# Kernel optimization log

Measured on AMD Instinct MI355X. Metric: run time of the kernel, lower is better.

## Reference

```python
import jax, jax.numpy as jnp
import numpy as np
import math

C, NH, HD, L, P, FFN = 256, 8, 32, 1, 4, 512
H_BEV, W_BEV = 200, 100
NQ, BS, NV = 1000, 4, H_BEV * W_BEV
EPS = 1e-5


def _ln(x, g, b):
    m = x.mean(-1, keepdims=True)
    v = ((x - m) ** 2).mean(-1, keepdims=True)
    return (x - m) / jnp.sqrt(v + EPS) * g + b


def _mha(x, qpos, in_w, in_b, ow, ob):
    # nn.MultiheadAttention self-attention; key_pos = query_pos (shapes match)
    q = x + qpos
    k = x + qpos
    v = x
    wq, wk, wv = jnp.split(in_w, 3, axis=0)
    bq, bk, bv = jnp.split(in_b, 3, axis=0)
    bs, nq, _ = x.shape
    qh = (q @ wq.T + bq).reshape(bs, nq, NH, HD)
    kh = (k @ wk.T + bk).reshape(bs, nq, NH, HD)
    vh = (v @ wv.T + bv).reshape(bs, nq, NH, HD)
    scores = jnp.einsum('bqhd,bkhd->bhqk', qh, kh) / jnp.sqrt(jnp.float32(HD))
    attn = jax.nn.softmax(scores, axis=-1)
    out = jnp.einsum('bhqk,bkhd->bqhd', attn, vh).reshape(bs, nq, C)
    return out @ ow.T + ob


def _msdeform(x, qpos, value, ref, spatial_shapes, so_w, so_b, aw_w, aw_b, vp_w, vp_b, op_w, op_b):
    # Multi-scale deformable attention (single level), bilinear sampling with
    # align_corners=False convention and zero padding, as in the CUDA kernel.
    bs, nq, _ = x.shape
    q = x + qpos
    v = (value @ vp_w.T + vp_b).reshape(bs, NV, NH, HD).transpose(0, 2, 1, 3)  # [bs,nh,nv,hd]
    off = (q @ so_w.T + so_b).reshape(bs, nq, NH, L, P, 2)
    aw = jax.nn.softmax((q @ aw_w.T + aw_b).reshape(bs, nq, NH, L * P), axis=-1)
    aw = aw.reshape(bs, nq, NH, L, P)
    norm = jnp.stack([spatial_shapes[:, 1], spatial_shapes[:, 0]], -1).astype(jnp.float32)  # [L,2] = (W,H)
    loc = ref[:, :, None, :, None, :] + off / norm[None, None, None, :, None, :]  # [bs,nq,nh,L,P,2]
    loc = loc[:, :, :, 0]  # single level -> [bs,nq,nh,P,2]
    awp = aw[:, :, :, 0]   # [bs,nq,nh,P]
    x_im = loc[..., 0] * W_BEV - 0.5
    y_im = loc[..., 1] * H_BEV - 0.5
    x0 = jnp.floor(x_im)
    y0 = jnp.floor(y_im)
    lx = x_im - x0
    ly = y_im - y0
    x0i = x0.astype(jnp.int32)
    y0i = y0.astype(jnp.int32)
    acc = jnp.zeros((bs, NH, nq, P, HD), jnp.float32)
    for dy in (0, 1):
        for dx in (0, 1):
            xi = x0i + dx
            yi = y0i + dy
            w = (lx if dx else 1.0 - lx) * (ly if dy else 1.0 - ly)  # [bs,nq,nh,P]
            ok = ((xi >= 0) & (xi < W_BEV) & (yi >= 0) & (yi < H_BEV)).astype(jnp.float32)
            idx = jnp.clip(yi, 0, H_BEV - 1) * W_BEV + jnp.clip(xi, 0, W_BEV - 1)
            idx_t = idx.transpose(0, 2, 1, 3).reshape(bs, NH, nq * P)
            g = jnp.take_along_axis(v, idx_t[..., None], axis=2).reshape(bs, NH, nq, P, HD)
            acc = acc + g * (w * ok).transpose(0, 2, 1, 3)[..., None]
    out = (acc * awp.transpose(0, 2, 1, 3)[..., None]).sum(3)  # [bs,nh,nq,hd]
    out = out.transpose(0, 2, 1, 3).reshape(bs, nq, C)
    return out @ op_w.T + op_b


def setup_inputs() -> dict:
    key = jax.random.key(0)
    ks = jax.random.split(key, 24)
    f32 = jnp.float32

    def w(k, shp):
        fan = shp[-1]
        return (jax.random.normal(k, shp, f32) * (1.0 / np.sqrt(fan))).astype(f32)

    # sampling_offsets bias per _reset_parameters (radial grid init)
    thetas = np.arange(NH, dtype=np.float32) * (2.0 * math.pi / NH)
    grid = np.stack([np.cos(thetas), np.sin(thetas)], -1)
    grid = grid / np.abs(grid).max(-1, keepdims=True)
    grid = np.tile(grid[:, None, None, :], (1, L, P, 1))
    for i in range(P):
        grid[:, :, i, :] *= i + 1
    so_b = jnp.asarray(grid.reshape(-1), f32)

    return {
        'query': jax.random.normal(ks[0], (NQ, BS, C), f32),
        'value': jax.random.normal(ks[1], (NV, BS, C), f32),
        'query_pos': jax.random.normal(ks[2], (NQ, BS, C), f32),
        'reference_points': jax.random.uniform(ks[3], (BS, NQ, L, 2), f32),
        'spatial_shapes': jnp.array([[H_BEV, W_BEV]], jnp.int32),
        'level_start_index': jnp.zeros((L,), jnp.int32),
        'in_proj_w': w(ks[4], (3 * C, C)),
        'in_proj_b': jnp.zeros((3 * C,), f32),
        'mha_ow': w(ks[5], (C, C)),
        'mha_ob': jnp.zeros((C,), f32),
        'so_w': w(ks[6], (NH * L * P * 2, C)) * 0.01,
        'so_b': so_b,
        'aw_w': w(ks[7], (NH * L * P, C)) * 0.01,
        'aw_b': jnp.zeros((NH * L * P,), f32),
        'vp_w': w(ks[8], (C, C)),
        'vp_b': jnp.zeros((C,), f32),
        'op_w': w(ks[9], (C, C)),
        'op_b': jnp.zeros((C,), f32),
        'ffn_w1': w(ks[10], (FFN, C)),
        'ffn_b1': jnp.zeros((FFN,), f32),
        'ffn_w2': w(ks[11], (C, FFN)),
        'ffn_b2': jnp.zeros((C,), f32),
        'ln1_g': jnp.ones((C,), f32), 'ln1_b': jnp.zeros((C,), f32),
        'ln2_g': jnp.ones((C,), f32), 'ln2_b': jnp.zeros((C,), f32),
        'ln3_g': jnp.ones((C,), f32), 'ln3_b': jnp.zeros((C,), f32),
    }


def reference(query, value, query_pos, reference_points, spatial_shapes, level_start_index,
              in_proj_w, in_proj_b, mha_ow, mha_ob, so_w, so_b, aw_w, aw_b,
              vp_w, vp_b, op_w, op_b, ffn_w1, ffn_b1, ffn_w2, ffn_b2,
              ln1_g, ln1_b, ln2_g, ln2_b, ln3_g, ln3_b):
    # batch_first=False: (seq, bs, C) -> (bs, seq, C)
    x = query.transpose(1, 0, 2)
    val = value.transpose(1, 0, 2)
    qpos = query_pos.transpose(1, 0, 2)
    # self_attn -> norm (residual inside attn wrapper; dropout=0 in eval)
    x = _ln(x + _mha(x, qpos, in_proj_w, in_proj_b, mha_ow, mha_ob), ln1_g, ln1_b)
    # cross_attn (MSDeformAttn) -> norm
    x = _ln(x + _msdeform(x, qpos, val, reference_points, spatial_shapes,
                          so_w, so_b, aw_w, aw_b, vp_w, vp_b, op_w, op_b), ln2_g, ln2_b)
    # ffn -> norm
    h = jax.nn.relu(x @ ffn_w1.T + ffn_b1) @ ffn_w2.T + ffn_b2
    x = _ln(x + h, ln3_g, ln3_b)
    return x.transpose(1, 0, 2)
```

## Files before the change

### kernel.cpp

```cpp
#include <hip/hip_runtime.h>
#include <hip/hip_bf16.h>
#include <cmath>

#define BS   4
#define NQ   1000
#define CDIM 256
#define NH   8
#define HD   32
#define NVAL 20000
#define FFND 512
#define PN   4
#define WBEV 100
#define HBEV 200
#define TK   64

typedef __bf16 v8bf __attribute__((ext_vector_type(8)));
typedef __bf16 v2bf __attribute__((ext_vector_type(2)));
typedef float  v4f  __attribute__((ext_vector_type(4)));

__device__ __forceinline__ void gload_lds16(const void* g, void* l) {
    __builtin_amdgcn_global_load_lds(
        (const __attribute__((address_space(1))) unsigned int*)g,
        (__attribute__((address_space(3))) unsigned int*)l, 16, 0, 0);
}

__global__ __launch_bounds__(256) void vgemm_kernel(
    const float* __restrict__ value, const __bf16* __restrict__ Wv,
    const float* __restrict__ bv, __bf16* __restrict__ vpj)
{
    __shared__ __align__(16) char smem[40960];
    __bf16* As = (__bf16*)smem;
    __bf16* Bs = (__bf16*)(smem + 8192);
    int tid = threadIdx.x;
    int wave = tid >> 6, lane = tid & 63, quad = lane >> 4, n16 = lane & 15;
    int bm = blockIdx.x * 64;
    int wm = (wave & 1) * 32, wn = (wave >> 1) * 128;
    v4f acc[2][8] = {};

    for (int k0 = 0; k0 < 256; k0 += 64) {
        float4 fa[2][2];
        #pragma unroll
        for (int i = 0; i < 2; i++) {
            int e = i * 256 + tid;
            int r = e >> 3, c = (e & 7) ^ (r & 7);
            const float* p = value + (long)(bm + r) * 256 + k0 + c * 8;
            fa[i][0] = *(const float4*)p;
            fa[i][1] = *(const float4*)(p + 4);
        }
        __syncthreads();
        #pragma unroll
        for (int i = 0; i < 2; i++) {
            int e = i * 256 + tid;
            v8bf v;
            v[0] = (__bf16)fa[i][0].x; v[1] = (__bf16)fa[i][0].y;
            v[2] = (__bf16)fa[i][0].z; v[3] = (__bf16)fa[i][0].w;
            v[4] = (__bf16)fa[i][1].x; v[5] = (__bf16)fa[i][1].y;
            v[6] = (__bf16)fa[i][1].z; v[7] = (__bf16)fa[i][1].w;
            *(v8bf*)(As + e * 8) = v;
        }
        #pragma unroll
        for (int i = 0; i < 8; i++) {
            int e = i * 256 + tid;
            int r = e >> 3, c = (e & 7) ^ (r & 7);
            gload_lds16(Wv + (long)r * 256 + k0 + c * 8, Bs + e * 8);
        }
        __syncthreads();
        #pragma unroll
        for (int s = 0; s < 2; s++) {
            v8bf af[2], bfr[8];
            #pragma unroll
            for (int mi = 0; mi < 2; mi++) {
                int row = wm + mi * 16 + n16;
                af[mi] = *(v8bf*)&As[row * 64 + (((quad + s * 4) ^ (row & 7))) * 8];
            }
            #pragma unroll
            for (int nj = 0; nj < 8; nj++) {
                int row = wn + nj * 16 + n16;
                bfr[nj] = *(v8bf*)&Bs[row * 64 + (((quad + s * 4) ^ (row & 7))) * 8];
            }
            #pragma unroll
            for (int mi = 0; mi < 2; mi++)
                #pragma unroll
                for (int nj = 0; nj < 8; nj++)
                    acc[mi][nj] = __builtin_amdgcn_mfma_f32_16x16x32_bf16(af[mi], bfr[nj], acc[mi][nj], 0, 0, 0);
        }
    }
    #pragma unroll
    for (int mi = 0; mi < 2; mi++) {
        #pragma unroll
        for (int r = 0; r < 4; r++) {
            int m = bm + wm + mi * 16 + quad * 4 + r;
            #pragma unroll
            for (int nj = 0; nj < 8; nj++) {
                int nn = wn + nj * 16 + n16;
                vpj[(long)m * 256 + nn] = (__bf16)(acc[mi][nj][r] + bv[nn]);
            }
        }
    }
}

__global__ __launch_bounds__(256) void prep_all_kernel(
    const float* __restrict__ query, const float* __restrict__ qpos,
    const float* __restrict__ in_w, const float* __restrict__ mha_ow,
    const float* __restrict__ vp_w, const float* __restrict__ op_w,
    const float* __restrict__ ffn_w1, const float* __restrict__ ffn_w2,
    const float* __restrict__ so_w, const float* __restrict__ aw_w,
    const float* __restrict__ so_b, const float* __restrict__ aw_b,
    float* __restrict__ x, float* __restrict__ qpos_t,
    __bf16* __restrict__ x_bf, __bf16* __restrict__ xq_bf,
    __bf16* __restrict__ wb, __bf16* __restrict__ wsmall,
    float* __restrict__ bsmall)
{
    int blk = blockIdx.x, tid = threadIdx.x;
    if (blk < 640) {
        long e = ((long)blk * 256 + tid) * 4;
        const float* src; long off;
        if      (e < 196608) { src = in_w;   off = e; }
        else if (e < 262144) { src = mha_ow; off = e - 196608; }
        else if (e < 327680) { src = vp_w;   off = e - 262144; }
        else if (e < 393216) { src = op_w;   off = e - 327680; }
        else if (e < 524288) { src = ffn_w1; off = e - 393216; }
        else                 { src = ffn_w2; off = e - 524288; }
        float4 v = *(const float4*)(src + off);
        __bf16* d = wb + e;
        d[0] = (__bf16)v.x; d[1] = (__bf16)v.y; d[2] = (__bf16)v.z; d[3] = (__bf16)v.w;
    } else if (blk < 4640) {
        int qb = blk - 640;
        int q = qb / BS, b = qb % BS;
        float qv = query[(q * BS + b) * CDIM + tid];
        float pv = qpos [(q * BS + b) * CDIM + tid];
        int o = (b * NQ + q) * CDIM + tid;
        x[o] = qv; qpos_t[o] = pv;
        x_bf[o] = (__bf16)qv; xq_bf[o] = (__bf16)(qv + pv);
    } else if (blk < 4672) {
        long e = ((long)(blk - 4640) * 256 + tid) * 4;
        int row = (int)(e >> 8), col = (int)(e & 255);
        float4 v = {0.f, 0.f, 0.f, 0.f};
        if (row < 64)      v = *(const float4*)(so_w + row * 256 + col);
        else if (row < 96) v = *(const float4*)(aw_w + (row - 64) * 256 + col);
        __bf16* d = wsmall + e;
        d[0] = (__bf16)v.x; d[1] = (__bf16)v.y; d[2] = (__bf16)v.z; d[3] = (__bf16)v.w;
    } else {
        if (tid < 128) bsmall[tid] = tid < 64 ? so_b[tid] : (tid < 96 ? aw_b[tid - 64] : 0.f);
    }
}

__global__ __launch_bounds__(256) void qkvv_kernel(
    const __bf16* __restrict__ xq, const __bf16* __restrict__ xv,
    const __bf16* __restrict__ W, const float* __restrict__ bias,
    __bf16* __restrict__ qk, __bf16* __restrict__ vh)
{
    __shared__ __align__(16) char smem[16384];
    int tid = threadIdx.x;
    int blk = blockIdx.x;
    int bn = (blk % 12) * 64, bm = (blk / 12) * 64;
    __bf16* As = (__bf16*)smem;
    __bf16* Bs = (__bf16*)(smem + 8192);
    const __bf16* A = (bn < 512) ? xq : xv;
    int wave = tid >> 6, lane = tid & 63, quad = lane >> 4, n16 = lane & 15;
    int wm = (wave & 1) * 32, wn = (wave >> 1) * 32;
    v4f acc[2][2] = {};

    for (int k0 = 0; k0 < 256; k0 += 64) {
        __syncthreads();
        #pragma unroll
        for (int i = 0; i < 2; i++) {
            int e = i * 256 + tid;
            int r = e >> 3, c = (e & 7) ^ (r & 7);
            int row = bm + r; if (row > BS * NQ - 1) row = BS * NQ - 1;
            gload_lds16(A + (long)row * 256 + k0 + c * 8, As + e * 8);
        }
        #pragma unroll
        for (int i = 0; i < 2; i++) {
            int e = i * 256 + tid;
            int r = e >> 3, c = (e & 7) ^ (r & 7);
            gload_lds16(W + (long)(bn + r) * 256 + k0 + c * 8, Bs + e * 8);
        }
        __syncthreads();
        #pragma unroll
        for (int s = 0; s < 2; s++) {
            v8bf af[2], bfr[2];
            #pragma unroll
            for (int mi = 0; mi < 2; mi++) {
                int row = wm + mi * 16 + n16;
                af[mi] = *(v8bf*)&As[row * 64 + (((quad + s * 4) ^ (row & 7))) * 8];
            }
            #pragma unroll
            for (int nj = 0; nj < 2; nj++) {
                int row = wn + nj * 16 + n16;
                bfr[nj] = *(v8bf*)&Bs[row * 64 + (((quad + s * 4) ^ (row & 7))) * 8];
            }
            #pragma unroll
            for (int mi = 0; mi < 2; mi++)
                #pragma unroll
                for (int nj = 0; nj < 2; nj++)
                    acc[mi][nj] = __builtin_amdgcn_mfma_f32_16x16x32_bf16(af[mi], bfr[nj], acc[mi][nj], 0, 0, 0);
        }
    }

    #pragma unroll
    for (int mi = 0; mi < 2; mi++) {
        #pragma unroll
        for (int r = 0; r < 4; r++) {
            int m = bm + wm + mi * 16 + quad * 4 + r;
            if (m >= BS * NQ) continue;
            #pragma unroll
            for (int nj = 0; nj < 2; nj++) {
                int nn = bn + wn + nj * 16 + n16;
                float v = acc[mi][nj][r] + bias[nn];
                if (nn < 512) qk[(long)m * 512 + nn] = (__bf16)v;
                else          vh[(long)m * 256 + (nn - 512)] = (__bf16)v;
            }
        }
    }
}

__global__ __launch_bounds__(256) void fattnv_kernel(
    const __bf16* __restrict__ qk, const __bf16* __restrict__ vh,
    __bf16* __restrict__ aout)
{
    __shared__ __align__(16) char smem[28672];
    int tid = threadIdx.x;
    int fb = blockIdx.x;
    int qt = fb & 15, h = (fb >> 4) & 7, b = fb >> 7;
    __bf16* Ks = (__bf16*)smem;
    __bf16* Vt = (__bf16*)(smem + 10240);
    __bf16* Pl = (__bf16*)(smem + 19456);
    int wave = tid >> 6, lane = tid & 63, quad = lane >> 4, n = lane & 15;
    int q0 = qt * 64 + wave * 16;
    const float scale = 0.17677669529663687f;
    const float M0 = 8.0f;

    int qrow = q0 + n; if (qrow > NQ - 1) qrow = NQ - 1;
    v8bf aq = *(const v8bf*)(qk + (long)(b * NQ + qrow) * 512 + h * HD + quad * 8);

    v4f o0 = {}, o1 = {};
    float lp[4] = {0.f, 0.f, 0.f, 0.f};

    int sv = tid >> 7;
    int t2 = tid & 127;
    int key = t2 & 63;
    int d16 = (t2 >> 6) * 16;

    v8bf stg0, stg1;
    auto loadtile = [&](int k0) {
        int krow = k0 + key; if (krow > NQ - 1) krow = NQ - 1;
        const __bf16* p = sv ? (vh + (long)(b * NQ + krow) * CDIM + h * HD + d16)
                             : (qk + (long)(b * NQ + krow) * 512 + 256 + h * HD + d16);
        stg0 = *(const v8bf*)p;
        stg1 = *(const v8bf*)(p + 8);
    };

    loadtile(0);
    int pb = 0;
    for (int k0 = 0; k0 < NQ; k0 += TK) {
        if (sv == 0) {
            *(v8bf*)&Ks[(pb * 64 + key) * 40 + d16]     = stg0;
            *(v8bf*)&Ks[(pb * 64 + key) * 40 + d16 + 8] = stg1;
        } else {
            #pragma unroll
            for (int j = 0; j < 8; j++) {
                Vt[(pb * 32 + d16 + j) * 72 + key]            = stg0[j];
                Vt[(pb * 32 + d16 + 8 + j) * 72 + (key ^ 16)] = stg1[j];
            }
        }
        if (k0 + TK < NQ) loadtile(k0 + TK);
        __syncthreads();

        v8bf bk0 = *(v8bf*)&Ks[(pb * 64 +      n) * 40 + quad * 8];
        v8bf bk1 = *(v8bf*)&Ks[(pb * 64 + 16 + n) * 40 + quad * 8];
        v8bf bk2 = *(v8bf*)&Ks[(pb * 64 + 32 + n) * 40 + quad * 8];
        v8bf bk3 = *(v8bf*)&Ks[(pb * 64 + 48 + n) * 40 + quad * 8];
        v4f z = {};
        v4f S0 = __builtin_amdgcn_mfma_f32_16x16x32_bf16(aq, bk0, z, 0, 0, 0);
        v4f S1 = __builtin_amdgcn_mfma_f32_16x16x32_bf16(aq, bk1, z, 0, 0, 0);
        v4f S2 = __builtin_amdgcn_mfma_f32_16x16x32_bf16(aq, bk2, z, 0, 0, 0);
        v4f S3 = __builtin_amdgcn_mfma_f32_16x16x32_bf16(aq, bk3, z, 0, 0, 0);

        bool last = (k0 + TK > NQ);
        float p0[4], p1[4], p2[4], p3[4];
        #pragma unroll
        for (int r = 0; r < 4; r++) {
            p0[r] = __expf(fmaf(S0[r], scale, -M0));
            p1[r] = __expf(fmaf(S1[r], scale, -M0));
            p2[r] = __expf(fmaf(S2[r], scale, -M0));
            p3[r] = __expf(fmaf(S3[r], scale, -M0));
            if (last) {
                if (k0 + 32 + n >= NQ) p2[r] = 0.f;
                if (k0 + 48 + n >= NQ) p3[r] = 0.f;
            }
            lp[r] += p0[r] + p1[r] + p2[r] + p3[r];
        }
        #pragma unroll
        for (int r = 0; r < 4; r++) {
            __bf16* pp = &Pl[(wave * 16 + quad * 4 + r) * 72];
            pp[n]      = (__bf16)p0[r];
            pp[16 + n] = (__bf16)p1[r];
            pp[32 + n] = (__bf16)p2[r];
            pp[48 + n] = (__bf16)p3[r];
        }
        asm volatile("s_waitcnt lgkmcnt(0)" ::: "memory");
        v8bf ap0 = *(v8bf*)&Pl[(wave * 16 + n) * 72 + quad * 8];
        v8bf ap1 = *(v8bf*)&Pl[(wave * 16 + n) * 72 + 32 + quad * 8];
        int swz = ((n >> 3) & 1) << 4;
        int c0 = (quad * 8) ^ swz;
        int c1 = (32 + quad * 8) ^ swz;
        v8bf bv00 = *(v8bf*)&Vt[(pb * 32 +      n) * 72 + c0];
        v8bf bv01 = *(v8bf*)&Vt[(pb * 32 +      n) * 72 + c1];
        v8bf bv10 = *(v8bf*)&Vt[(pb * 32 + 16 + n) * 72 + c0];
        v8bf bv11 = *(v8bf*)&Vt[(pb * 32 + 16 + n) * 72 + c1];
        o0 = __builtin_amdgcn_mfma_f32_16x16x32_bf16(ap0, bv00, o0, 0, 0, 0);
        o0 = __builtin_amdgcn_mfma_f32_16x16x32_bf16(ap1, bv01, o0, 0, 0, 0);
        o1 = __builtin_amdgcn_mfma_f32_16x16x32_bf16(ap0, bv10, o1, 0, 0, 0);
        o1 = __builtin_amdgcn_mfma_f32_16x16x32_bf16(ap1, bv11, o1, 0, 0, 0);
        pb ^= 1;
    }

    #pragma unroll
    for (int r = 0; r < 4; r++) {
        float l = lp[r];
        #pragma unroll
        for (int off = 1; off < 16; off <<= 1) l += __shfl_xor(l, off, 16);
        int q = q0 + quad * 4 + r;
        if (q < NQ) {
            float invl = 1.0f / l;
            __bf16* op = aout + ((long)(b * NQ + q) * CDIM + h * HD);
            op[n]      = (__bf16)(o0[r] * invl);
            op[16 + n] = (__bf16)(o1[r] * invl);
        }
    }
}

__global__ __launch_bounds__(256) void gln1s_kernel(
    const __bf16* __restrict__ A, const __bf16* __restrict__ W,
    const float* __restrict__ bias, const float* __restrict__ res,
    const float* __restrict__ g, const float* __restrict__ beta,
    const float* __restrict__ qpos_t,
    const __bf16* __restrict__ Wsm, const float* __restrict__ bsm,
    float* __restrict__ outf, float* __restrict__ soawO)
{
    __shared__ __align__(16) char smem[43776];
    int tid = threadIdx.x;
    __bf16* As  = (__bf16*)smem;
    __bf16* Bs  = (__bf16*)(smem + 2048);
    __bf16* Axq = (__bf16*)(smem + 34816);
    float* redS = (float*)(smem + 43264);
    float* redQ = redS + 64;
    int bm = blockIdx.x * 16;
    int wave = tid >> 6, lane = tid & 63, quad = lane >> 4, n16 = lane & 15;
    int wn = wave * 64;
    v4f acc[4] = {};

    for (int k0 = 0; k0 < 256; k0 += 64) {
        __syncthreads();
        if (tid < 128) {
            int e = tid;
            int r = e >> 3, c = (e & 7) ^ (r & 7);
            gload_lds16(A + (long)(bm + r) * 256 + k0 + c * 8, As + e * 8);
        }
        #pragma unroll
        for (int i = 0; i < 8; i++) {
            int e = i * 256 + tid;
            int r = e >> 3, c = (e & 7) ^ (r & 7);
            gload_lds16(W + (long)r * 256 + k0 + c * 8, Bs + e * 8);
        }
        __syncthreads();
        #pragma unroll
        for (int s = 0; s < 2; s++) {
            v8bf af = *(v8bf*)&As[n16 * 64 + (((quad + s * 4) ^ (n16 & 7))) * 8];
            #pragma unroll
            for (int nj = 0; nj < 4; nj++) {
                int row = wn + nj * 16 + n16;
                v8bf bfr = *(v8bf*)&Bs[row * 64 + (((quad + s * 4) ^ (row & 7))) * 8];
                acc[nj] = __builtin_amdgcn_mfma_f32_16x16x32_bf16(af, bfr, acc[nj], 0, 0, 0);
            }
        }
    }

    float y[4][4], s1[4] = {}, s2[4] = {};
    #pragma unroll
    for (int r = 0; r < 4; r++) {
        int m = bm + quad * 4 + r;
        #pragma unroll
        for (int nj = 0; nj < 4; nj++) {
            int nn = wn + nj * 16 + n16;
            float v = acc[nj][r] + bias[nn] + res[(long)m * 256 + nn];
            y[r][nj] = v;
            s1[r] += v; s2[r] += v * v;
        }
    }
    #pragma unroll
    for (int r = 0; r < 4; r++) {
        #pragma unroll
        for (int off = 1; off < 16; off <<= 1) {
            s1[r] += __shfl_xor(s1[r], off, 16);
            s2[r] += __shfl_xor(s2[r], off, 16);
        }
    }
    if (n16 == 0) {
        #pragma unroll
        for (int r = 0; r < 4; r++) {
            redS[wave * 16 + quad * 4 + r] = s1[r];
            redQ[wave * 16 + quad * 4 + r] = s2[r];
        }
    }
    __syncthreads();
    #pragma unroll
    for (int r = 0; r < 4; r++) {
        int mr = quad * 4 + r;
        float ts = redS[mr] + redS[16 + mr] + redS[32 + mr] + redS[48 + mr];
        float tq = redQ[mr] + redQ[16 + mr] + redQ[32 + mr] + redQ[48 + mr];
        float mean = ts * (1.0f / 256.0f);
        float var = tq * (1.0f / 256.0f) - mean * mean;
        float rinv = rsqrtf(var + 1e-5f);
        int m = bm + mr;
        #pragma unroll
        for (int nj = 0; nj < 4; nj++) {
            int nn = wn + nj * 16 + n16;
            float o = (y[r][nj] - mean) * rinv * g[nn] + beta[nn];
            outf[(long)m * 256 + nn] = o;
            Axq[mr * 264 + nn] = (__bf16)(o + qpos_t[(long)m * 256 + nn]);
        }
    }
    __syncthreads();
    if (wave < 3) {
        v4f sacc[2] = {};
        #pragma unroll
        for (int k0 = 0; k0 < 256; k0 += 32) {
            v8bf af = *(v8bf*)&Axq[n16 * 264 + k0 + quad * 8];
            #pragma unroll
            for (int t = 0; t < 2; t++) {
                int col = wave * 32 + t * 16 + n16;
                v8bf bw = *(const v8bf*)(Wsm + (long)col * 256 + k0 + quad * 8);
                sacc[t] = __builtin_amdgcn_mfma_f32_16x16x32_bf16(af, bw, sacc[t], 0, 0, 0);
            }
        }
        #pragma unroll
        for (int t = 0; t < 2; t++)
            #pragma unroll
            for (int r = 0; r < 4; r++) {
                int mm = bm + quad * 4 + r;
                int col = wave * 32 + t * 16 + n16;
                soawO[(long)mm * 96 + col] = sacc[t][r] + bsm[col];
            }
    }
}

__global__ __launch_bounds__(256) void msds_kernel(
    const __bf16* __restrict__ vproj, const float* __restrict__ soaw,
    const float* __restrict__ refp, __bf16* __restrict__ out)
{
    int t = threadIdx.x;
    int bq = blockIdx.x * 2 + (t >> 7);
    int b = bq / NQ; int q = bq % NQ;
    int t2 = t & 127;
    int h = t2 >> 4;
    int d0 = (t2 & 15) * 2;
    float rx = refp[(b * NQ + q) * 2 + 0];
    float ry = refp[(b * NQ + q) * 2 + 1];
    const float* rowp = soaw + (long)(b * NQ + q) * 96;
    const float* offp = rowp + h * 8;
    const float* awp  = rowp + 64 + h * 4;
    float a0 = awp[0], a1 = awp[1], a2 = awp[2], a3 = awp[3];
    float m = fmaxf(fmaxf(a0, a1), fmaxf(a2, a3));
    float e0 = __expf(a0 - m), e1 = __expf(a1 - m), e2 = __expf(a2 - m), e3 = __expf(a3 - m);
    float invs = 1.0f / (e0 + e1 + e2 + e3);
    float accA = 0.f, accB = 0.f;
    #pragma unroll
    for (int p = 0; p < PN; p++) {
        float ew = (p == 0 ? e0 : p == 1 ? e1 : p == 2 ? e2 : e3) * invs;
        float xim = rx * (float)WBEV + offp[p * 2 + 0] - 0.5f;
        float yim = ry * (float)HBEV + offp[p * 2 + 1] - 0.5f;
        float x0f = floorf(xim), y0f = floorf(yim);
        float lx = xim - x0f, ly = yim - y0f;
        int x0 = (int)x0f, y0 = (int)y0f;
        float gA = 0.f, gB = 0.f;
        #pragma unroll
        for (int dy = 0; dy < 2; dy++) {
            #pragma unroll
            for (int dx = 0; dx < 2; dx++) {
                int xi = x0 + dx, yi = y0 + dy;
                float w = (dx ? lx : 1.f - lx) * (dy ? ly : 1.f - ly);
                bool ok = (xi >= 0 && xi < WBEV && yi >= 0 && yi < HBEV);
                int xc = min(max(xi, 0), WBEV - 1);
                int yc = min(max(yi, 0), HBEV - 1);
                int idx = yc * WBEV + xc;
                v2bf gv = *(const v2bf*)(vproj + ((long)(idx * BS + b)) * CDIM + h * HD + d0);
                float wk = (ok ? w : 0.f);
                gA += wk * (float)gv[0];
                gB += wk * (float)gv[1];
            }
        }
        accA += ew * gA;
        accB += ew * gB;
    }
    v2bf o2; o2[0] = (__bf16)accA; o2[1] = (__bf16)accB;
    *(v2bf*)(out + (long)(b * NQ + q) * CDIM + h * HD + d0) = o2;
}

__global__ __launch_bounds__(512) void gtail_kernel(
    const __bf16* __restrict__ A, const __bf16* __restrict__ Wop,
    const float* __restrict__ opb, const float* __restrict__ res,
    const float* __restrict__ g2, const float* __restrict__ b2ln,
    const __bf16* __restrict__ W1, const float* __restrict__ b1,
    const __bf16* __restrict__ W2, const float* __restrict__ bff2,
    const float* __restrict__ g3, const float* __restrict__ b3ln,
    float* __restrict__ outf)
{
    __shared__ __align__(16) char smem[60416];
    __bf16* As  = (__bf16*)smem;
    __bf16* Bs  = (__bf16*)(smem + 2048);
    __bf16* As2 = (__bf16*)(smem + 34816);
    __bf16* h1s = (__bf16*)(smem + 43008);
    float* redS = (float*)(smem + 59392);
    float* redQ = (float*)(smem + 59904);
    int tid = threadIdx.x;
    int bm = blockIdx.x * 16;
    int wave = tid >> 6, lane = tid & 63, quad = lane >> 4, n16 = lane & 15;
    int wn = wave * 32;
    int mr_ = quad * 4;

    v4f acc[2] = {};
    for (int k0 = 0; k0 < 256; k0 += 64) {
        __syncthreads();
        if (tid < 128) {
            int e = tid;
            int r = e >> 3, c = (e & 7) ^ (r & 7);
            gload_lds16(A + (long)(bm + r) * 256 + k0 + c * 8, As + e * 8);
        }
        #pragma unroll
        for (int i = 0; i < 4; i++) {
            int e = i * 512 + tid;
            int r = e >> 3, c = (e & 7) ^ (r & 7);
            gload_lds16(Wop + (long)r * 256 + k0 + c * 8, Bs + e * 8);
        }
        __syncthreads();
        #pragma unroll
        for (int s = 0; s < 2; s++) {
            v8bf af = *(v8bf*)&As[n16 * 64 + (((quad + s * 4) ^ (n16 & 7))) * 8];
            #pragma unroll
            for (int nj = 0; nj < 2; nj++) {
                int row = wn + nj * 16 + n16;
                v8bf bfr = *(v8bf*)&Bs[row * 64 + (((quad + s * 4) ^ (row & 7))) * 8];
                acc[nj] = __builtin_amdgcn_mfma_f32_16x16x32_bf16(af, bfr, acc[nj], 0, 0, 0);
            }
        }
    }
    float yv[4][2], s1[4] = {}, s2[4] = {};
    #pragma unroll
    for (int r = 0; r < 4; r++) {
        int m = bm + mr_ + r;
        #pragma unroll
        for (int nj = 0; nj < 2; nj++) {
            int nn = wn + nj * 16 + n16;
            float v = acc[nj][r] + opb[nn] + res[(long)m * 256 + nn];
            yv[r][nj] = v;
            s1[r] += v; s2[r] += v * v;
        }
    }
    #pragma unroll
    for (int r = 0; r < 4; r++) {
        #pragma unroll
        for (int off = 1; off < 16; off <<= 1) {
            s1[r] += __shfl_xor(s1[r], off, 16);
            s2[r] += __shfl_xor(s2[r], off, 16);
        }
    }
    if (n16 == 0) {
        #pragma unroll
        for (int r = 0; r < 4; r++) {
            redS[wave * 16 + mr_ + r] = s1[r];
            redQ[wave * 16 + mr_ + r] = s2[r];
        }
    }
    __syncthreads();
    #pragma unroll
    for (int r = 0; r < 4; r++) {
        int mr = mr_ + r;
        float ts = 0.f, tq = 0.f;
        #pragma unroll
        for (int j = 0; j < 8; j++) { ts += redS[j * 16 + mr]; tq += redQ[j * 16 + mr]; }
        float mean = ts * (1.0f / 256.0f);
        float var = tq * (1.0f / 256.0f) - mean * mean;
        float rinv = rsqrtf(var + 1e-5f);
        #pragma unroll
        for (int nj = 0; nj < 2; nj++) {
            int nn = wn + nj * 16 + n16;
            float o = (yv[r][nj] - mean) * rinv * g2[nn] + b2ln[nn];
            yv[r][nj] = o;
            int kc = nn >> 6, c6 = nn & 63;
            As2[kc * 1024 + mr * 64 + (((c6 >> 3) ^ (mr & 7)) << 3) + (c6 & 7)] = (__bf16)o;
        }
    }

    #pragma unroll 1
    for (int H = 0; H < 2; H++) {
        v4f accB[2] = {};
        for (int k0 = 0; k0 < 256; k0 += 64) {
            __syncthreads();
            #pragma unroll
            for (int i = 0; i < 4; i++) {
                int e = i * 512 + tid;
                int r = e >> 3, c = (e & 7) ^ (r & 7);
                gload_lds16(W1 + (long)(H * 256 + r) * 256 + k0 + c * 8, Bs + e * 8);
            }
            __syncthreads();
            int kc = k0 >> 6;
            #pragma unroll
            for (int s = 0; s < 2; s++) {
                v8bf af = *(v8bf*)&As2[kc * 1024 + n16 * 64 + (((quad + s * 4) ^ (n16 & 7))) * 8];
                #pragma unroll
                for (int nj = 0; nj < 2; nj++) {
                    int row = wn + nj * 16 + n16;
                    v8bf bfr = *(v8bf*)&Bs[row * 64 + (((quad + s * 4) ^ (row & 7))) * 8];
                    accB[nj] = __builtin_amdgcn_mfma_f32_16x16x32_bf16(af, bfr, accB[nj], 0, 0, 0);
                }
            }
        }
        #pragma unroll
        for (int r = 0; r < 4; r++) {
            int mr = mr_ + r;
            #pragma unroll
            for (int nj = 0; nj < 2; nj++) {
                int col = H * 256 + wn + nj * 16 + n16;
                float v = accB[nj][r] + b1[col];
                v = fmaxf(v, 0.f);
                int kc = col >> 6, c6 = col & 63;
                h1s[kc * 1024 + mr * 64 + (((c6 >> 3) ^ (mr & 7)) << 3) + (c6 & 7)] = (__bf16)v;
            }
        }
    }

    v4f acc3[2] = {};
    for (int k0 = 0; k0 < 512; k0 += 64) {
        __syncthreads();
        #pragma unroll
        for (int i = 0; i < 4; i++) {
            int e = i * 512 + tid;
            int r = e >> 3, c = (e & 7) ^ (r & 7);
            gload_lds16(W2 + (long)r * 512 + k0 + c * 8, Bs + e * 8);
        }
        __syncthreads();
        int kc = k0 >> 6;
        #pragma unroll
        for (int s = 0; s < 2; s++) {
            v8bf af = *(v8bf*)&h1s[kc * 1024 + n16 * 64 + (((quad + s * 4) ^ (n16 & 7))) * 8];
            #pragma unroll
            for (int nj = 0; nj < 2; nj++) {
                int row = wn + nj * 16 + n16;
                v8bf bfr = *(v8bf*)&Bs[row * 64 + (((quad + s * 4) ^ (row & 7))) * 8];
                acc3[nj] = __builtin_amdgcn_mfma_f32_16x16x32_bf16(af, bfr, acc3[nj], 0, 0, 0);
            }
        }
    }
    float y3[4][2], t1[4] = {}, t2[4] = {};
    #pragma unroll
    for (int r = 0; r < 4; r++) {
        #pragma unroll
        for (int nj = 0; nj < 2; nj++) {
            int nn = wn + nj * 16 + n16;
            float v = acc3[nj][r] + bff2[nn] + yv[r][nj];
            y3[r][nj] = v;
            t1[r] += v; t2[r] += v * v;
        }
    }
    #pragma unroll
    for (int r = 0; r < 4; r++) {
        #pragma unroll
        for (int off = 1; off < 16; off <<= 1) {
            t1[r] += __shfl_xor(t1[r], off, 16);
            t2[r] += __shfl_xor(t2[r], off, 16);
        }
    }
    __syncthreads();
    if (n16 == 0) {
        #pragma unroll
        for (int r = 0; r < 4; r++) {
            redS[wave * 16 + mr_ + r] = t1[r];
            redQ[wave * 16 + mr_ + r] = t2[r];
        }
    }
    __syncthreads();
    #pragma unroll
    for (int r = 0; r < 4; r++) {
        int mr = mr_ + r;
        float ts = 0.f, tq = 0.f;
        #pragma unroll
        for (int j = 0; j < 8; j++) { ts += redS[j * 16 + mr]; tq += redQ[j * 16 + mr]; }
        float mean = ts * (1.0f / 256.0f);
        float var = tq * (1.0f / 256.0f) - mean * mean;
        float rinv = rsqrtf(var + 1e-5f);
        int m = bm + mr;
        int b = m / NQ, q = m - b * NQ;
        #pragma unroll
        for (int nj = 0; nj < 2; nj++) {
            int nn = wn + nj * 16 + n16;
            float o = (y3[r][nj] - mean) * rinv * g3[nn] + b3ln[nn];
            outf[(long)(q * BS + b) * 256 + nn] = o;
        }
    }
}

extern "C" void kernel_launch(void* const* d_in, const int* in_sizes, int n_in,
                              void* d_out, int out_size, void* d_ws, size_t ws_size,
                              hipStream_t stream) {
    const float* query = (const float*)d_in[0];
    const float* value = (const float*)d_in[1];
    const float* qpos  = (const float*)d_in[2];
    const float* refp  = (const float*)d_in[3];
    const float* in_w  = (const float*)d_in[6];
    const float* in_b  = (const float*)d_in[7];
    const float* mha_ow = (const float*)d_in[8];
    const float* mha_ob = (const float*)d_in[9];
    const float* so_w  = (const float*)d_in[10];
    const float* so_b  = (const float*)d_in[11];
    const float* aw_w  = (const float*)d_in[12];
    const float* aw_b  = (const float*)d_in[13];
    const float* vp_w  = (const float*)d_in[14];
    const float* vp_b  = (const float*)d_in[15];
    const float* op_w  = (const float*)d_in[16];
    const float* op_b  = (const float*)d_in[17];
    const float* ffn_w1 = (const float*)d_in[18];
    const float* ffn_b1 = (const float*)d_in[19];
    const float* ffn_w2 = (const float*)d_in[20];
    const float* ffn_b2 = (const float*)d_in[21];
    const float* ln1_g = (const float*)d_in[22];
    const float* ln1_b = (const float*)d_in[23];
    const float* ln2_g = (const float*)d_in[24];
    const float* ln2_b = (const float*)d_in[25];
    const float* ln3_g = (const float*)d_in[26];
    const float* ln3_b = (const float*)d_in[27];
    float* out = (float*)d_out;

    const long NTOK = (long)BS * NQ * CDIM;

    float* x      = (float*)d_ws;
    float* qpos_t = x + NTOK;
    float* x1     = qpos_t + NTOK;
    float* x2     = x1 + NTOK;
    float* soaw   = x2 + NTOK;
    float* bsmall = soaw + (long)BS * NQ * 96;
    __bf16* x_bf   = (__bf16*)(bsmall + 128);
    __bf16* xq_bf  = x_bf + NTOK;
    __bf16* qk_bf  = xq_bf + NTOK;
    __bf16* vh_bf  = qk_bf + 2 * NTOK;
    __bf16* aA_bf  = vh_bf + NTOK;
    __bf16* x2_bf  = aA_bf + NTOK;
    __bf16* h1_bf  = x2_bf + NTOK;
    __bf16* vpj_bf = h1_bf + 2 * NTOK;
    __bf16* wb     = vpj_bf + (long)BS * NVAL * CDIM;
    __bf16* inw_b  = wb;
    __bf16* mow_b  = wb + 196608;
    __bf16* vpw_b  = wb + 262144;
    __bf16* opw_b  = wb + 327680;
    __bf16* fw1_b  = wb + 393216;
    __bf16* fw2_b  = wb + 524288;
    __bf16* wsmall = wb + 655360;

    dim3 blk(256);

    prep_all_kernel<<<4673, blk, 0, stream>>>(
        query, qpos, in_w, mha_ow, vp_w, op_w, ffn_w1, ffn_w2,
        so_w, aw_w, so_b, aw_b,
        x, qpos_t, x_bf, xq_bf, wb, wsmall, bsmall);

    qkvv_kernel<<<756, blk, 0, stream>>>(xq_bf, x_bf, inw_b, in_b, qk_bf, vh_bf);

    vgemm_kernel<<<1250, blk, 0, stream>>>(value, vpw_b, vp_b, vpj_bf);

    fattnv_kernel<<<512, blk, 0, stream>>>(qk_bf, vh_bf, aA_bf);

    gln1s_kernel<<<250, blk, 0, stream>>>(
        aA_bf, mow_b, mha_ob, x, ln1_g, ln1_b, qpos_t, wsmall, bsmall,
        x1, soaw);

    msds_kernel<<<2000, blk, 0, stream>>>(vpj_bf, soaw, refp, aA_bf);

    gtail_kernel<<<250, dim3(512), 0, stream>>>(
        aA_bf, opw_b, op_b, x1, ln2_g, ln2_b,
        fw1_b, ffn_b1, fw2_b, ffn_b2, ln3_g, ln3_b, out);
}
```

Baseline: 264.3 us.

## Merge value GEMM into QKV launch and split attention over keys

Folds the value-projection GEMM blocks into the QKV projection kernel as extra blocks, so the two independent GEMMs share one launch and can fill the GPU together. Splits the self-attention key range into two halves, doubling the block count. Each half writes unnormalized fp32 partial outputs and row sums, which the following out-projection kernel sums and normalizes while loading its A tile. The split relies on the fixed max offset M0 rather than a running max. In exchange it adds fp32 partial-buffer traffic, a non-async A load in gln1s, and raises the QKV kernel's LDS to 40 KB, which may lower its occupancy.

```diff
diff --git a/kernel.cpp b/kernel.cpp
--- a/kernel.cpp
+++ b/kernel.cpp
@@ -24,16 +24,15 @@
         (__attribute__((address_space(3))) unsigned int*)l, 16, 0, 0);
 }
 
-__global__ __launch_bounds__(256) void vgemm_kernel(
-    const float* __restrict__ value, const __bf16* __restrict__ Wv,
-    const float* __restrict__ bv, __bf16* __restrict__ vpj)
+__device__ __forceinline__ void vgemm64_block(
+    int vb, const float* __restrict__ value, const __bf16* __restrict__ Wv,
+    const float* __restrict__ bv, __bf16* __restrict__ vpj, char* smem)
 {
-    __shared__ __align__(16) char smem[40960];
     __bf16* As = (__bf16*)smem;
     __bf16* Bs = (__bf16*)(smem + 8192);
     int tid = threadIdx.x;
     int wave = tid >> 6, lane = tid & 63, quad = lane >> 4, n16 = lane & 15;
-    int bm = blockIdx.x * 64;
+    int bm = vb * 64;
     int wm = (wave & 1) * 32, wn = (wave >> 1) * 128;
     v4f acc[2][8] = {};
 
@@ -148,10 +147,16 @@
 __global__ __launch_bounds__(256) void qkvv_kernel(
     const __bf16* __restrict__ xq, const __bf16* __restrict__ xv,
     const __bf16* __restrict__ W, const float* __restrict__ bias,
-    __bf16* __restrict__ qk, __bf16* __restrict__ vh)
+    __bf16* __restrict__ qk, __bf16* __restrict__ vh,
+    const float* __restrict__ value, const __bf16* __restrict__ Wv,
+    const float* __restrict__ bv, __bf16* __restrict__ vpj)
 {
-    __shared__ __align__(16) char smem[16384];
+    __shared__ __align__(16) char smem[40960];
     int tid = threadIdx.x;
+    if ((int)blockIdx.x >= 756) {
+        vgemm64_block(blockIdx.x - 756, value, Wv, bv, vpj, smem);
+        return;
+    }
     int blk = blockIdx.x;
     int bn = (blk % 12) * 64, bm = (blk / 12) * 64;
     __bf16* As = (__bf16*)smem;
@@ -215,14 +220,16 @@
     }
 }
 
-__global__ __launch_bounds__(256) void fattnv_kernel(
+__global__ __launch_bounds__(256) void fattns_kernel(
     const __bf16* __restrict__ qk, const __bf16* __restrict__ vh,
-    __bf16* __restrict__ aout)
+    float* __restrict__ op0, float* __restrict__ op1, float* __restrict__ lpart)
 {
     __shared__ __align__(16) char smem[28672];
     int tid = threadIdx.x;
     int fb = blockIdx.x;
-    int qt = fb & 15, h = (fb >> 4) & 7, b = fb >> 7;
+    int split = fb >> 9;
+    int f2 = fb & 511;
+    int qt = f2 & 15, h = (f2 >> 4) & 7, b = f2 >> 7;
     __bf16* Ks = (__bf16*)smem;
     __bf16* Vt = (__bf16*)(smem + 10240);
     __bf16* Pl = (__bf16*)(smem + 19456);
@@ -251,9 +258,11 @@
         stg1 = *(const v8bf*)(p + 8);
     };
 
-    loadtile(0);
+    int kstart = split * 512;
+    int kend = split ? NQ : 512;
+    loadtile(kstart);
     int pb = 0;
-    for (int k0 = 0; k0 < NQ; k0 += TK) {
+    for (int k0 = kstart; k0 < kend; k0 += TK) {
         if (sv == 0) {
             *(v8bf*)&Ks[(pb * 64 + key) * 40 + d16]     = stg0;
             *(v8bf*)&Ks[(pb * 64 + key) * 40 + d16 + 8] = stg1;
@@ -264,7 +273,7 @@
                 Vt[(pb * 32 + d16 + 8 + j) * 72 + (key ^ 16)] = stg1[j];
             }
         }
-        if (k0 + TK < NQ) loadtile(k0 + TK);
+        if (k0 + TK < kend) loadtile(k0 + TK);
         __syncthreads();
 
         v8bf bk0 = *(v8bf*)&Ks[(pb * 64 +      n) * 40 + quad * 8];
@@ -316,6 +325,7 @@
         pb ^= 1;
     }
 
+    float* oP = split ? op1 : op0;
     #pragma unroll
     for (int r = 0; r < 4; r++) {
         float l = lp[r];
@@ -323,16 +333,18 @@
         for (int off = 1; off < 16; off <<= 1) l += __shfl_xor(l, off, 16);
         int q = q0 + quad * 4 + r;
         if (q < NQ) {
-            float invl = 1.0f / l;
-            __bf16* op = aout + ((long)(b * NQ + q) * CDIM + h * HD);
-            op[n]      = (__bf16)(o0[r] * invl);
-            op[16 + n] = (__bf16)(o1[r] * invl);
+            float* opp = oP + (long)(b * NQ + q) * 256 + h * HD;
+            opp[n]      = o0[r];
+            opp[16 + n] = o1[r];
+            if (n == 0) lpart[split * 32000 + (b * NQ + q) * 8 + h] = l;
         }
     }
 }
 
 __global__ __launch_bounds__(256) void gln1s_kernel(
-    const __bf16* __restrict__ A, const __bf16* __restrict__ W,
+    const float* __restrict__ op0, const float* __restrict__ op1,
+    const float* __restrict__ lpart,
+    const __bf16* __restrict__ W,
     const float* __restrict__ bias, const float* __restrict__ res,
     const float* __restrict__ g, const float* __restrict__ beta,
     const float* __restrict__ qpos_t,
@@ -355,8 +367,27 @@
         __syncthreads();
         if (tid < 128) {
             int e = tid;
-            int r = e >> 3, c = (e & 7) ^ (r & 7);
-            gload_lds16(A + (long)(bm + r) * 256 + k0 + c * 8, As + e * 8);
+            int r = e >> 3, c8 = (e & 7) ^ (r & 7);
+            int m = bm + r;
+            int col = k0 + c8 * 8;
+            int hh = col >> 5;
+            float invl = 1.0f / (lpart[m * 8 + hh] + lpart[32000 + m * 8 + hh]);
+            const float* p0 = op0 + (long)m * 256 + col;
+            const float* p1 = op1 + (long)m * 256 + col;
+            float4 a0 = *(const float4*)p0;
+            float4 a1 = *(const float4*)(p0 + 4);
+            float4 b0 = *(const float4*)p1;
+            float4 b1 = *(const float4*)(p1 + 4);
+            v8bf v;
+            v[0] = (__bf16)((a0.x + b0.x) * invl);
+            v[1] = (__bf16)((a0.y + b0.y) * invl);
+            v[2] = (__bf16)((a0.z + b0.z) * invl);
+            v[3] = (__bf16)((a0.w + b0.w) * invl);
+            v[4] = (__bf16)((a1.x + b1.x) * invl);
+            v[5] = (__bf16)((a1.y + b1.y) * invl);
+            v[6] = (__bf16)((a1.z + b1.z) * invl);
+            v[7] = (__bf16)((a1.w + b1.w) * invl);
+            *(v8bf*)(As + e * 8) = v;
         }
         #pragma unroll
         for (int i = 0; i < 8; i++) {
@@ -757,6 +788,10 @@
     __bf16* fw2_b  = wb + 524288;
     __bf16* wsmall = wb + 655360;
 
+    float* opart0 = x2;
+    float* opart1 = (float*)h1_bf;
+    float* lpart  = (float*)x2_bf;
+
     dim3 blk(256);
 
     prep_all_kernel<<<4673, blk, 0, stream>>>(
@@ -764,15 +799,14 @@
         so_w, aw_w, so_b, aw_b,
         x, qpos_t, x_bf, xq_bf, wb, wsmall, bsmall);
 
-    qkvv_kernel<<<756, blk, 0, stream>>>(xq_bf, x_bf, inw_b, in_b, qk_bf, vh_bf);
-
-    vgemm_kernel<<<1250, blk, 0, stream>>>(value, vpw_b, vp_b, vpj_bf);
-
-    fattnv_kernel<<<512, blk, 0, stream>>>(qk_bf, vh_bf, aA_bf);
+    qkvv_kernel<<<2006, blk, 0, stream>>>(xq_bf, x_bf, inw_b, in_b, qk_bf, vh_bf,
+                                          value, vpw_b, vp_b, vpj_bf);
+
+    fattns_kernel<<<1024, blk, 0, stream>>>(qk_bf, vh_bf, opart0, opart1, lpart);
 
     gln1s_kernel<<<250, blk, 0, stream>>>(
-        aA_bf, mow_b, mha_ob, x, ln1_g, ln1_b, qpos_t, wsmall, bsmall,
-        x1, soaw);
+        opart0, opart1, lpart, mow_b, mha_ob, x, ln1_g, ln1_b, qpos_t,
+        wsmall, bsmall, x1, soaw);
 
     msds_kernel<<<2000, blk, 0, stream>>>(vpj_bf, soaw, refp, aA_bf);
 
```

Measured after the change: 261.1 us. About the same (-1.2%).
